# Kernel optimization log

Hardware: AMD Instinct MI355X
Metric: run time of the kernel (lower is better)

Reference implementation:

```python
import jax, jax.numpy as jnp
import numpy as np

# --- reconstructed config / key constants (from init_kwargs) ---
SCALES = (8, 16, 32)                      # patch sizes tiling H, W
TEMPORAL_WINDOWS = (0, 250, 500, 750, 1000)
KEY_INT = 0x5D1CE5                        # deterministic int derived from watermark_key+model_id
BASE_STRENGTH = 0.05
HASH_MOD = 10007
TWO_PI = 6.2831853


def _watermark_bias_map(latent, timestep):
    """Vectorized equivalent of the per-scale / per-patch Python loops.

    For each scale p: tile HxW into (H/p)x(W/p) patches, pool latent over
    (batch, channel, patch) -> scalar per patch, combine with a keyed integer
    hash phase into g in [-1,1], scale by a per-(scale,timestep) strength, and
    paint the constant bias over each patch region (the spatial mask).
    Returns a [H, W] bias map broadcastable over [B, C, H, W].
    """
    B, C, H, W = latent.shape
    # temporal bucket (timestep is a static Python int)
    bucket = int(np.searchsorted(np.asarray(TEMPORAL_WINDOWS), timestep, side='right') - 1)
    total = jnp.zeros((H, W), dtype=latent.dtype)
    for p in SCALES:
        gh, gw = H // p, W // p
        # pooled features per patch: mean over batch, channels, and patch pixels -> [gh, gw]
        pooled = latent.reshape(B, C, gh, p, gw, p).mean(axis=(0, 1, 3, 5))
        # keyed hash phase per patch (top-left coords i*p, j*p)
        base = (KEY_INT * 2654435761 + p * 97 + bucket * 139) % HASH_MOD
        i = (jnp.arange(gh, dtype=jnp.int32) * (p * 131))[:, None]
        j = (jnp.arange(gw, dtype=jnp.int32) * (p * 137))[None, :]
        h = (base + i + j) % HASH_MOD                           # [gh, gw] int
        phase = h.astype(latent.dtype) * (TWO_PI / HASH_MOD)
        g = jnp.cos(pooled * 3.0 + phase)                       # g_value in [-1, 1]
        strength = np.float32(BASE_STRENGTH / np.sqrt(p) * np.exp(-timestep / 1000.0))
        # broadcast patch-constant bias over the full spatial mask region
        total = total + jnp.repeat(jnp.repeat(g * strength, p, axis=0), p, axis=1)
    return total


def setup_inputs() -> dict:
    key = jax.random.key(0)
    k1, k2 = jax.random.split(key)
    B, C, H, W = 64, 4, 256, 256
    noise = jax.random.normal(k1, (B, C, H, W), dtype=jnp.float32)
    latent = jax.random.normal(k2, (B, C, H, W), dtype=jnp.float32)
    return {"noise": noise, "latent": latent, "timestep": 500}


def reference(noise, latent, timestep):
    bias = _watermark_bias_map(latent, timestep)        # [H, W]
    return noise + bias[None, None, :, :]               # [B, C, H, W]
```

## Files before the change

kernel.cpp:

```cpp
#include <hip/hip_runtime.h>
#include <hip/hip_bf16.h>

static constexpr unsigned long long KEY_MUL =
    (6102245ULL * 2654435761ULL) % 10007ULL;
static constexpr int HASH_MOD = 10007;
static constexpr float TWO_PI = 6.2831853f;

__global__ __launch_bounds__(256) void pool_kernel(
    const float* __restrict__ latent, float* __restrict__ ws_sum) {
  const int pr  = blockIdx.y;
  const int pc0 = blockIdx.x;
  const int t   = threadIdx.x;
  const int cl  = t & 63;
  const int rg  = t >> 6;

  float acc = 0.0f;
  const float4* base = reinterpret_cast<const float4*>(latent);
  for (int pl = 0; pl < 8; ++pl) {
    const size_t plane = (size_t)(pc0 * 8 + pl);
    const float4* prow = base + plane * 16384;
#pragma unroll
    for (int rr = 0; rr < 2; ++rr) {
      const int r = pr * 8 + rg + rr * 4;
      float4 v = prow[r * 64 + cl];
      acc += v.x + v.y + v.z + v.w;
    }
  }
  acc += __shfl_xor(acc, 1, 64);

  __shared__ float lds[4][32];
  if ((cl & 1) == 0) lds[rg][cl >> 1] = acc;
  __syncthreads();
  if (t < 32) {
    float s = lds[0][t] + lds[1][t] + lds[2][t] + lds[3][t];
    atomicAdd(&ws_sum[pr * 32 + t], s);
  }
}

__global__ __launch_bounds__(1024) void gmap_kernel(
    const float* __restrict__ ws_sum, const int* __restrict__ tstep,
    float* __restrict__ gtab) {
  const int t = threadIdx.x;
  const int ts = *tstep;

  int bucket = -1;
  const int wins[5] = {0, 250, 500, 750, 1000};
#pragma unroll
  for (int k = 0; k < 5; ++k) bucket += (ts >= wins[k]) ? 1 : 0;

  const double expo = exp(-(double)ts / 1000.0);
  const float phase_k = (float)(6.2831853 / 10007.0);

  {
    const int p = 8;
    const int i = t >> 5, j = t & 31;
    const long long b =
        ((long long)KEY_MUL + p * 97 + bucket * 139 + 10 * HASH_MOD) % HASH_MOD;
    const int h = (int)((b + (long long)i * (p * 131) + (long long)j * (p * 137)) % HASH_MOD);
    const float pooled = ws_sum[t] * (1.0f / 16384.0f);
    const float strength = (float)(0.05 / sqrt((double)p) * expo);
    gtab[t] = cosf(pooled * 3.0f + (float)h * phase_k) * strength;
  }
  if (t < 256) {
    const int p = 16;
    const int i = t >> 4, j = t & 15;
    const long long b =
        ((long long)KEY_MUL + p * 97 + bucket * 139 + 10 * HASH_MOD) % HASH_MOD;
    const int h = (int)((b + (long long)i * (p * 131) + (long long)j * (p * 137)) % HASH_MOD);
    const float s =
        ws_sum[(2 * i) * 32 + 2 * j] + ws_sum[(2 * i) * 32 + 2 * j + 1] +
        ws_sum[(2 * i + 1) * 32 + 2 * j] + ws_sum[(2 * i + 1) * 32 + 2 * j + 1];
    const float pooled = s * (1.0f / 65536.0f);
    const float strength = (float)(0.05 / sqrt((double)p) * expo);
    gtab[1024 + t] = cosf(pooled * 3.0f + (float)h * phase_k) * strength;
  }
  if (t < 64) {
    const int p = 32;
    const int i = t >> 3, j = t & 7;
    const long long b =
        ((long long)KEY_MUL + p * 97 + bucket * 139 + 10 * HASH_MOD) % HASH_MOD;
    const int h = (int)((b + (long long)i * (p * 131) + (long long)j * (p * 137)) % HASH_MOD);
    float s = 0.0f;
    for (int di = 0; di < 4; ++di)
      for (int dj = 0; dj < 4; ++dj)
        s += ws_sum[(4 * i + di) * 32 + 4 * j + dj];
    const float pooled = s * (1.0f / 262144.0f);
    const float strength = (float)(0.05 / sqrt((double)p) * expo);
    gtab[1280 + t] = cosf(pooled * 3.0f + (float)h * phase_k) * strength;
  }
}

__global__ __launch_bounds__(256) void add_kernel(
    const float* __restrict__ noise, const float* __restrict__ gtab,
    float* __restrict__ out) {
  __shared__ float g8[1024];
  __shared__ float g16[256];
  __shared__ float g32[64];
  for (int i = threadIdx.x; i < 1344; i += blockDim.x) {
    float v = gtab[i];
    if (i < 1024) g8[i] = v;
    else if (i < 1280) g16[i - 1024] = v;
    else g32[i - 1280] = v;
  }
  __syncthreads();

  const float4* __restrict__ n4 = reinterpret_cast<const float4*>(noise);
  float4* __restrict__ o4 = reinterpret_cast<float4*>(out);
  const int total4 = 64 * 4 * 256 * 256 / 4;
  const int stride = gridDim.x * blockDim.x;
  for (int f = blockIdx.x * blockDim.x + threadIdx.x; f < total4; f += stride) {
    const int fp = f & 16383;
    const int h = fp >> 6;
    const int wq = fp & 63;
    const float bias = g8[(h >> 3) * 32 + (wq >> 1)] +
                       g16[(h >> 4) * 16 + (wq >> 2)] +
                       g32[(h >> 5) * 8 + (wq >> 3)];
    float4 v = n4[f];
    v.x += bias; v.y += bias; v.z += bias; v.w += bias;
    o4[f] = v;
  }
}

extern "C" void kernel_launch(void* const* d_in, const int* in_sizes, int n_in,
                              void* d_out, int out_size, void* d_ws, size_t ws_size,
                              hipStream_t stream) {
  const float* noise  = (const float*)d_in[0];
  const float* latent = (const float*)d_in[1];
  const int*   tstep  = (const int*)d_in[2];
  float* out = (float*)d_out;
  float* ws  = (float*)d_ws;

  float* ws_sum = ws;
  float* gtab   = ws + 1024;

  hipMemsetAsync(ws_sum, 0, 1024 * sizeof(float), stream);
  pool_kernel<<<dim3(32, 32), 256, 0, stream>>>(latent, ws_sum);
  gmap_kernel<<<1, 1024, 0, stream>>>(ws_sum, tstep, gtab);
  add_kernel<<<2048, 256, 0, stream>>>(noise, gtab, out);
}
```

Baseline: 45.22 us.

## Replace atomic pooling with per-chunk partials and unroll add kernel loads

The pool kernel now writes per-chunk partial sums to distinct workspace slots instead of using atomicAdd. This removes the memset launch and the atomic contention, and gmap_kernel reduces the partials into shared memory. The add kernel drops its grid-stride loop: each block handles exactly 2048 float4s, issuing eight loads up front and computing biases from hoisted column indices. The fixed mapping assumes the grid exactly covers the tensor, and the launcher selects a chunk count based on workspace size.

New measurement: 43.02 us. -4.9%, faster.

```diff
diff --git a/kernel.cpp b/kernel.cpp
--- a/kernel.cpp
+++ b/kernel.cpp
@@ -4,26 +4,26 @@
 static constexpr unsigned long long KEY_MUL =
     (6102245ULL * 2654435761ULL) % 10007ULL;
 static constexpr int HASH_MOD = 10007;
-static constexpr float TWO_PI = 6.2831853f;
 
+template <int NCH>
 __global__ __launch_bounds__(256) void pool_kernel(
-    const float* __restrict__ latent, float* __restrict__ ws_sum) {
-  const int pr  = blockIdx.y;
-  const int pc0 = blockIdx.x;
-  const int t   = threadIdx.x;
-  const int cl  = t & 63;
-  const int rg  = t >> 6;
+    const float* __restrict__ latent, float* __restrict__ ws_partial) {
+  constexpr int PPC = 256 / NCH;
+  const int pr = blockIdx.y;
+  const int ch = blockIdx.x;
+  const int t  = threadIdx.x;
+  const int cl = t & 63;
+  const int rg = t >> 6;
 
   float acc = 0.0f;
   const float4* base = reinterpret_cast<const float4*>(latent);
-  for (int pl = 0; pl < 8; ++pl) {
-    const size_t plane = (size_t)(pc0 * 8 + pl);
-    const float4* prow = base + plane * 16384;
+#pragma unroll 8
+  for (int pl = 0; pl < PPC; ++pl) {
+    const float4* prow = base + (size_t)(ch * PPC + pl) * 16384;
 #pragma unroll
     for (int rr = 0; rr < 2; ++rr) {
-      const int r = pr * 8 + rg + rr * 4;
-      float4 v = prow[r * 64 + cl];
-      acc += v.x + v.y + v.z + v.w;
+      float4 v = prow[(pr * 8 + rg + rr * 4) * 64 + cl];
+      acc += (v.x + v.y) + (v.z + v.w);
     }
   }
   acc += __shfl_xor(acc, 1, 64);
@@ -32,17 +32,35 @@
   if ((cl & 1) == 0) lds[rg][cl >> 1] = acc;
   __syncthreads();
   if (t < 32) {
-    float s = lds[0][t] + lds[1][t] + lds[2][t] + lds[3][t];
-    atomicAdd(&ws_sum[pr * 32 + t], s);
+    float s = (lds[0][t] + lds[1][t]) + (lds[2][t] + lds[3][t]);
+    ws_partial[(pr * 32 + t) * NCH + ch] = s;
   }
 }
 
+template <int NCH>
 __global__ __launch_bounds__(1024) void gmap_kernel(
-    const float* __restrict__ ws_sum, const int* __restrict__ tstep,
+    const float* __restrict__ ws_partial, const int* __restrict__ tstep,
     float* __restrict__ gtab) {
+  __shared__ float s8[1024];
   const int t = threadIdx.x;
+  {
+    float s = 0.0f;
+    if constexpr (NCH >= 4) {
+      const float4* p4 = reinterpret_cast<const float4*>(ws_partial) + t * (NCH / 4);
+#pragma unroll
+      for (int c = 0; c < NCH / 4; ++c) {
+        float4 v = p4[c];
+        s += (v.x + v.y) + (v.z + v.w);
+      }
+    } else {
+#pragma unroll
+      for (int c = 0; c < NCH; ++c) s += ws_partial[t * NCH + c];
+    }
+    s8[t] = s;
+  }
+  __syncthreads();
+
   const int ts = *tstep;
-
   int bucket = -1;
   const int wins[5] = {0, 250, 500, 750, 1000};
 #pragma unroll
@@ -52,38 +70,35 @@
   const float phase_k = (float)(6.2831853 / 10007.0);
 
   {
-    const int p = 8;
-    const int i = t >> 5, j = t & 31;
+    const int p = 8, i = t >> 5, j = t & 31;
     const long long b =
         ((long long)KEY_MUL + p * 97 + bucket * 139 + 10 * HASH_MOD) % HASH_MOD;
     const int h = (int)((b + (long long)i * (p * 131) + (long long)j * (p * 137)) % HASH_MOD);
-    const float pooled = ws_sum[t] * (1.0f / 16384.0f);
+    const float pooled = s8[t] * (1.0f / 16384.0f);
     const float strength = (float)(0.05 / sqrt((double)p) * expo);
     gtab[t] = cosf(pooled * 3.0f + (float)h * phase_k) * strength;
   }
   if (t < 256) {
-    const int p = 16;
-    const int i = t >> 4, j = t & 15;
+    const int p = 16, i = t >> 4, j = t & 15;
     const long long b =
         ((long long)KEY_MUL + p * 97 + bucket * 139 + 10 * HASH_MOD) % HASH_MOD;
     const int h = (int)((b + (long long)i * (p * 131) + (long long)j * (p * 137)) % HASH_MOD);
-    const float s =
-        ws_sum[(2 * i) * 32 + 2 * j] + ws_sum[(2 * i) * 32 + 2 * j + 1] +
-        ws_sum[(2 * i + 1) * 32 + 2 * j] + ws_sum[(2 * i + 1) * 32 + 2 * j + 1];
+    const float s = (s8[(2 * i) * 32 + 2 * j] + s8[(2 * i) * 32 + 2 * j + 1]) +
+                    (s8[(2 * i + 1) * 32 + 2 * j] + s8[(2 * i + 1) * 32 + 2 * j + 1]);
     const float pooled = s * (1.0f / 65536.0f);
     const float strength = (float)(0.05 / sqrt((double)p) * expo);
     gtab[1024 + t] = cosf(pooled * 3.0f + (float)h * phase_k) * strength;
   }
   if (t < 64) {
-    const int p = 32;
-    const int i = t >> 3, j = t & 7;
+    const int p = 32, i = t >> 3, j = t & 7;
     const long long b =
         ((long long)KEY_MUL + p * 97 + bucket * 139 + 10 * HASH_MOD) % HASH_MOD;
     const int h = (int)((b + (long long)i * (p * 131) + (long long)j * (p * 137)) % HASH_MOD);
     float s = 0.0f;
+#pragma unroll
     for (int di = 0; di < 4; ++di)
-      for (int dj = 0; dj < 4; ++dj)
-        s += ws_sum[(4 * i + di) * 32 + 4 * j + dj];
+#pragma unroll
+      for (int dj = 0; dj < 4; ++dj) s += s8[(4 * i + di) * 32 + 4 * j + dj];
     const float pooled = s * (1.0f / 262144.0f);
     const float strength = (float)(0.05 / sqrt((double)p) * expo);
     gtab[1280 + t] = cosf(pooled * 3.0f + (float)h * phase_k) * strength;
@@ -96,7 +111,8 @@
   __shared__ float g8[1024];
   __shared__ float g16[256];
   __shared__ float g32[64];
-  for (int i = threadIdx.x; i < 1344; i += blockDim.x) {
+  const int t = threadIdx.x;
+  for (int i = t; i < 1344; i += 256) {
     float v = gtab[i];
     if (i < 1024) g8[i] = v;
     else if (i < 1280) g16[i - 1024] = v;
@@ -104,20 +120,32 @@
   }
   __syncthreads();
 
+  const int b = blockIdx.x;
+  const size_t f_base = (size_t)b * 2048 + t;
+  const int o = b & 7;
+  const int c8 = (t & 63) >> 1, c16 = (t & 63) >> 2, c32 = (t & 63) >> 3;
+  const int h0 = o * 32 + (t >> 6);
+
   const float4* __restrict__ n4 = reinterpret_cast<const float4*>(noise);
   float4* __restrict__ o4 = reinterpret_cast<float4*>(out);
-  const int total4 = 64 * 4 * 256 * 256 / 4;
-  const int stride = gridDim.x * blockDim.x;
-  for (int f = blockIdx.x * blockDim.x + threadIdx.x; f < total4; f += stride) {
-    const int fp = f & 16383;
-    const int h = fp >> 6;
-    const int wq = fp & 63;
-    const float bias = g8[(h >> 3) * 32 + (wq >> 1)] +
-                       g16[(h >> 4) * 16 + (wq >> 2)] +
-                       g32[(h >> 5) * 8 + (wq >> 3)];
-    float4 v = n4[f];
-    v.x += bias; v.y += bias; v.z += bias; v.w += bias;
-    o4[f] = v;
+
+  float4 v[8];
+#pragma unroll
+  for (int k = 0; k < 8; ++k) v[k] = n4[f_base + (size_t)k * 256];
+
+  float bias[8];
+#pragma unroll
+  for (int k = 0; k < 8; ++k) {
+    const int h = h0 + k * 4;
+    bias[k] = g8[(h >> 3) * 32 + c8] + g16[(h >> 4) * 16 + c16] +
+              g32[(h >> 5) * 8 + c32];
+  }
+
+#pragma unroll
+  for (int k = 0; k < 8; ++k) {
+    float4 w = v[k];
+    w.x += bias[k]; w.y += bias[k]; w.z += bias[k]; w.w += bias[k];
+    o4[f_base + (size_t)k * 256] = w;
   }
 }
 
@@ -130,11 +158,22 @@
   float* out = (float*)d_out;
   float* ws  = (float*)d_ws;
 
-  float* ws_sum = ws;
-  float* gtab   = ws + 1024;
+  const size_t need32 = (size_t)(1024 * 32 + 1344) * sizeof(float);
+  const size_t need8  = (size_t)(1024 * 8 + 1344) * sizeof(float);
 
-  hipMemsetAsync(ws_sum, 0, 1024 * sizeof(float), stream);
-  pool_kernel<<<dim3(32, 32), 256, 0, stream>>>(latent, ws_sum);
-  gmap_kernel<<<1, 1024, 0, stream>>>(ws_sum, tstep, gtab);
+  float* gtab;
+  if (ws_size >= need32) {
+    float* part = ws; gtab = ws + 1024 * 32;
+    pool_kernel<32><<<dim3(32, 32), 256, 0, stream>>>(latent, part);
+    gmap_kernel<32><<<1, 1024, 0, stream>>>(part, tstep, gtab);
+  } else if (ws_size >= need8) {
+    float* part = ws; gtab = ws + 1024 * 8;
+    pool_kernel<8><<<dim3(8, 32), 256, 0, stream>>>(latent, part);
+    gmap_kernel<8><<<1, 1024, 0, stream>>>(part, tstep, gtab);
+  } else {
+    float* part = ws; gtab = ws + 1024;
+    pool_kernel<1><<<dim3(1, 32), 256, 0, stream>>>(latent, part);
+    gmap_kernel<1><<<1, 1024, 0, stream>>>(part, tstep, gtab);
+  }
   add_kernel<<<2048, 256, 0, stream>>>(noise, gtab, out);
 }
```
